# Optimization experiments

Measured on AMD Instinct MI355X. Metric: run time of the kernel, lower is better.

Reference implementation:

```python
import jax, jax.numpy as jnp
import numpy as np
import math

B, N0, IW, HW, OW, EG, DEPTH = 8, 16384, 128, 128, 2, 98304, 4
RATIO = 0.8


def setup_inputs() -> dict:
    key = jax.random.key(0)
    ks = list(jax.random.split(key, 40))
    inp = {
        "x": jax.random.normal(ks[0], (B, N0, IW), jnp.float32),
        "src": jax.random.randint(ks[1], (B, EG), 0, N0, jnp.int32),
        "dst": jax.random.randint(ks[2], (B, EG), 0, N0, jnp.int32),
    }
    def lin(k, fi, fo):
        return jax.random.normal(k, (fi, fo), jnp.float32) / np.sqrt(fi).astype(np.float32)
    j = 3
    for i in range(DEPTH):
        cin = IW if i == 0 else HW
        inp[f"c{i}_w1"] = lin(ks[j], cin, cin); j += 1
        inp[f"c{i}_b1"] = jnp.zeros((cin,), jnp.float32)
        inp[f"c{i}_w2"] = lin(ks[j], cin, HW); j += 1
        inp[f"c{i}_b2"] = jnp.zeros((HW,), jnp.float32)
        inp[f"p{i}_w"] = jax.random.normal(ks[j], (HW,), jnp.float32); j += 1
    inp["q1_w"] = lin(ks[j], 2 * HW, HW); j += 1
    inp["q1_b"] = jnp.zeros((HW,), jnp.float32)
    inp["q2_w"] = lin(ks[j], HW, HW // 2); j += 1
    inp["q2_b"] = jnp.zeros((HW // 2,), jnp.float32)
    inp["q3_w"] = lin(ks[j], HW // 2, OW); j += 1
    inp["q3_b"] = jnp.zeros((OW,), jnp.float32)
    return inp


def _forward(x, src, dst, conv_params, pool_ws, q1_w, q1_b, q2_w, q2_b, q3_w, q3_b):
    bidx = jnp.arange(B)[:, None]
    emask = jnp.ones(src.shape, x.dtype)  # edge validity mask (replaces PyG filter_adj)
    readouts = []
    for i in range(DEPTH):
        w1, b1, w2, b2 = conv_params[i]
        pw = pool_ws[i]
        # --- GINConv (eps=0, sum aggregation): MLP(x + sum_{j->i} x_j) ---
        msg = jnp.take_along_axis(x, src[:, :, None], axis=1) * emask[:, :, None]  # [B,E,C]
        agg = jnp.zeros_like(x).at[bidx, dst].add(msg)
        h = x + agg
        h = jax.nn.relu(h @ w1 + b1)
        x = jax.nn.relu(h @ w2 + b2)  # [B,n,HW]
        # --- TopKPooling(ratio=0.8, nonlinearity=tanh) ---
        n = x.shape[1]
        k = math.ceil(RATIO * n)
        score = jnp.tanh((x @ pw) / jnp.linalg.norm(pw))  # [B,n]
        vals, idx = jax.lax.top_k(score, k)  # per-graph top-k (descending)
        x = jnp.take_along_axis(x, idx[:, :, None], axis=1) * vals[:, :, None]  # [B,k,HW]
        # re-index edges: old node id -> new id (or -1 if dropped)
        mapping = jnp.full((B, n), -1, jnp.int32).at[bidx, idx].set(
            jnp.broadcast_to(jnp.arange(k, dtype=jnp.int32), (B, k)))
        nsrc = jnp.take_along_axis(mapping, src, axis=1)
        ndst = jnp.take_along_axis(mapping, dst, axis=1)
        valid = (nsrc >= 0) & (ndst >= 0) & (emask > 0)
        src = jnp.where(valid, nsrc, 0)
        dst = jnp.where(valid, ndst, 0)
        emask = valid.astype(x.dtype)
        # --- readout: [global_max_pool, global_mean_pool] ---
        readouts.append(jnp.concatenate([x.max(axis=1), x.mean(axis=1)], axis=1))
    r = readouts[0]
    for t in readouts[1:]:
        r = r + t  # sum over depth of stacked readouts
    # predictor (Dropout is identity in eval)
    h = jax.nn.relu(r @ q1_w + q1_b)
    h = jax.nn.relu(h @ q2_w + q2_b)
    return h @ q3_w + q3_b


def reference(x, src, dst,
              c0_w1, c0_b1, c0_w2, c0_b2, p0_w,
              c1_w1, c1_b1, c1_w2, c1_b2, p1_w,
              c2_w1, c2_b1, c2_w2, c2_b2, p2_w,
              c3_w1, c3_b1, c3_w2, c3_b2, p3_w,
              q1_w, q1_b, q2_w, q2_b, q3_w, q3_b):
    conv_params = [(c0_w1, c0_b1, c0_w2, c0_b2), (c1_w1, c1_b1, c1_w2, c1_b2),
                   (c2_w1, c2_b1, c2_w2, c2_b2), (c3_w1, c3_b1, c3_w2, c3_b2)]
    pool_ws = [p0_w, p1_w, p2_w, p3_w]
    return _forward(x, src, dst, conv_params, pool_ws, q1_w, q1_b, q2_w, q2_b, q3_w, q3_b)
```

## Files before the change

### kernel.cpp

```cpp
#include <hip/hip_runtime.h>
#include <math.h>

#define NB 8
#define N0 16384
#define NC 128
#define NE 98304

typedef unsigned short ushort_t;
using short8 = __attribute__((ext_vector_type(8))) short;
using f32x4 = __attribute__((ext_vector_type(4))) float;

__device__ __forceinline__ unsigned mono_u(float f) {
  unsigned u = __float_as_uint(f);
  return (u & 0x80000000u) ? ~u : (u | 0x80000000u);
}
__device__ __forceinline__ int f2ikey(float f) {
  int i = __float_as_int(f);
  return (i >= 0) ? i : (i ^ 0x7fffffff);
}
__device__ __forceinline__ float ikey2f(int k) {
  return __int_as_float(k >= 0 ? k : (k ^ 0x7fffffff));
}
__device__ __forceinline__ ushort_t f2bf_rne(float f) {
  unsigned u = __float_as_uint(f);
  unsigned r = u + 0x7fffu + ((u >> 16) & 1u);
  return (ushort_t)(r >> 16);
}
__device__ __forceinline__ int wscan_incl(int v, int lane) {
#pragma unroll
  for (int o = 1; o < 64; o <<= 1) {
    int u = __shfl_up(v, o);
    if (lane >= o) v += u;
  }
  return v;
}

__global__ void k_init(const int* __restrict__ src, const int* __restrict__ dst,
                       int* __restrict__ srcw, int* __restrict__ dstw,
                       int* __restrict__ cnt, int* __restrict__ maxbuf, float* __restrict__ sumbuf) {
  int stride = gridDim.x * blockDim.x;
  int i = blockIdx.x * blockDim.x + threadIdx.x;
  for (int j = i; j < NB * NE; j += stride) {
    int d = dst[j];
    srcw[j] = src[j];
    dstw[j] = d;
    atomicAdd(&cnt[(j / NE) * N0 + d], 1);
  }
  for (int j = i; j < 4 * NB * NC; j += stride) {
    maxbuf[j] = (int)0x80000000;
    sumbuf[j] = 0.f;
  }
}

__global__ void k_wprep(const float* __restrict__ W, ushort_t* __restrict__ Wt) {
  int id = blockIdx.x * blockDim.x + threadIdx.x;
  if (id >= NC * NC) return;
  int k = id >> 7, c = id & 127;
  Wt[c * NC + k] = f2bf_rne(W[id]);
}

__global__ __launch_bounds__(1024) void k_scan(int* __restrict__ cnt,
                                               int* __restrict__ offs, int* __restrict__ cursor) {
  __shared__ int wsum[16];
  int b = blockIdx.x, t = threadIdx.x, lane = t & 63, wid = t >> 6;
  int base = b * N0 + t * 16;
  int loc[16];
  int s = 0;
#pragma unroll
  for (int j = 0; j < 16; j++) { loc[j] = cnt[base + j]; s += loc[j]; cnt[base + j] = 0; }
  int incl = wscan_incl(s, lane);
  if (lane == 63) wsum[wid] = incl;
  __syncthreads();
  int woff = 0;
  for (int w = 0; w < wid; w++) woff += wsum[w];
  int excl = woff + incl - s;
#pragma unroll
  for (int j = 0; j < 16; j++) {
    offs[base + j] = excl;
    cursor[base + j] = excl;
    excl += loc[j];
  }
}

__global__ void k_fill(const int* __restrict__ srcw, const int* __restrict__ dstw,
                       int* __restrict__ cursor, int* __restrict__ elist) {
  int tot = NB * NE;
  for (int i = blockIdx.x * blockDim.x + threadIdx.x; i < tot; i += gridDim.x * blockDim.x) {
    int d = dstw[i];
    if (d < 0) continue;
    int b = i / NE;
    int pos = atomicAdd(&cursor[b * N0 + d], 1);
    elist[b * NE + pos] = srcw[i];
  }
}

__global__ void k_gather(const float* __restrict__ X, ushort_t* __restrict__ H,
                         const int* __restrict__ offs, const int* __restrict__ cend,
                         const int* __restrict__ elist, int n) {
  int b = blockIdx.x & 7;
  int chunk = blockIdx.x >> 3;
  int lane = threadIdx.x & 63, wid = threadIdx.x >> 6;
  int node = chunk * 4 + wid;
  if (node >= n) return;
  int off = offs[b * N0 + node];
  int deg = cend[b * N0 + node] - off;
  int h = lane >> 5, c4 = lane & 31;
  const float* Xb = X + (size_t)b * N0 * NC;

  float4 acc0 = make_float4(0.f, 0.f, 0.f, 0.f);
  float4 acc1 = make_float4(0.f, 0.f, 0.f, 0.f);
  if (h == 0) acc0 = *reinterpret_cast<const float4*>(&Xb[(size_t)node * NC + c4 * 4]);

  for (int base = 0; base < deg; base += 64) {
    int m = min(64, deg - base);
    int eid = (lane < m) ? elist[b * NE + off + base + lane] : 0;
    int j = 0;
    for (; j + 4 <= m; j += 4) {
      int s0 = __shfl(eid, j + h);
      int s1 = __shfl(eid, j + 2 + h);
      float4 v0 = *reinterpret_cast<const float4*>(&Xb[(size_t)s0 * NC + c4 * 4]);
      float4 v1 = *reinterpret_cast<const float4*>(&Xb[(size_t)s1 * NC + c4 * 4]);
      acc0.x += v0.x; acc0.y += v0.y; acc0.z += v0.z; acc0.w += v0.w;
      acc1.x += v1.x; acc1.y += v1.y; acc1.z += v1.z; acc1.w += v1.w;
    }
    if (j + 2 <= m) {
      int s0 = __shfl(eid, j + h);
      float4 v0 = *reinterpret_cast<const float4*>(&Xb[(size_t)s0 * NC + c4 * 4]);
      acc0.x += v0.x; acc0.y += v0.y; acc0.z += v0.z; acc0.w += v0.w;
      j += 2;
    }
    if (j < m) {
      int s0 = __shfl(eid, j);
      if (h == 0) {
        float4 v0 = *reinterpret_cast<const float4*>(&Xb[(size_t)s0 * NC + c4 * 4]);
        acc0.x += v0.x; acc0.y += v0.y; acc0.z += v0.z; acc0.w += v0.w;
      }
    }
  }
  acc0.x += acc1.x; acc0.y += acc1.y; acc0.z += acc1.z; acc0.w += acc1.w;
  acc0.x += __shfl_xor(acc0.x, 32);
  acc0.y += __shfl_xor(acc0.y, 32);
  acc0.z += __shfl_xor(acc0.z, 32);
  acc0.w += __shfl_xor(acc0.w, 32);
  if (h == 0) {
    unsigned p0 = (unsigned)f2bf_rne(acc0.x) | ((unsigned)f2bf_rne(acc0.y) << 16);
    unsigned p1 = (unsigned)f2bf_rne(acc0.z) | ((unsigned)f2bf_rne(acc0.w) << 16);
    *reinterpret_cast<uint2*>(&H[((size_t)b * N0 + node) * NC + c4 * 4]) = make_uint2(p0, p1);
  }
}

__global__ __launch_bounds__(256) void k_gin(const ushort_t* __restrict__ Xh,
                                             float* __restrict__ Xout,
                                             const ushort_t* __restrict__ W1t,
                                             const float* __restrict__ b1,
                                             const ushort_t* __restrict__ W2t,
                                             const float* __restrict__ b2,
                                             const float* __restrict__ pw,
                                             float* __restrict__ score, int n) {
  __shared__ ushort_t Ts[128 * 136];
  __shared__ ushort_t Wsh[128 * 136];
  int b = blockIdx.x & 7;
  int r0 = (blockIdx.x >> 3) * 128;
  int t = threadIdx.x;
  const ushort_t* Xg = Xh + (size_t)b * N0 * NC;

#pragma unroll
  for (int p = 0; p < 8; p++) {
    int id = t + p * 256;
    int row = id >> 4, seg = id & 15;
    short8 vh = (short8)0;
    if (r0 + row < n)
      vh = *reinterpret_cast<const short8*>(&Xg[(size_t)(r0 + row) * NC + seg * 8]);
    *reinterpret_cast<short8*>(&Ts[row * 136 + seg * 8]) = vh;
    *reinterpret_cast<short8*>(&Wsh[row * 136 + seg * 8]) =
        *reinterpret_cast<const short8*>(&W1t[row * NC + seg * 8]);
  }
  __syncthreads();

  int lane = t & 63, w = t >> 6;
  int li = lane & 15, lg = lane >> 4;
  int rbase = w * 32;

  f32x4 acc[2][8];
#pragma unroll
  for (int rt = 0; rt < 2; rt++)
#pragma unroll
    for (int ct = 0; ct < 8; ct++) acc[rt][ct] = (f32x4)0.f;

#pragma unroll
  for (int ks = 0; ks < 4; ks++) {
    short8 x0 = *reinterpret_cast<const short8*>(&Ts[(rbase + li) * 136 + ks * 32 + lg * 8]);
    short8 x1 = *reinterpret_cast<const short8*>(&Ts[(rbase + 16 + li) * 136 + ks * 32 + lg * 8]);
#pragma unroll
    for (int ct = 0; ct < 8; ct++) {
      short8 wf = *reinterpret_cast<const short8*>(&Wsh[(ct * 16 + li) * 136 + ks * 32 + lg * 8]);
      acc[0][ct] = __builtin_amdgcn_mfma_f32_16x16x32_bf16(wf, x0, acc[0][ct], 0, 0, 0);
      acc[1][ct] = __builtin_amdgcn_mfma_f32_16x16x32_bf16(wf, x1, acc[1][ct], 0, 0, 0);
    }
  }

#pragma unroll
  for (int rt = 0; rt < 2; rt++) {
    int row = rbase + rt * 16 + li;
#pragma unroll
    for (int ct = 0; ct < 8; ct++) {
      float4 bq = *reinterpret_cast<const float4*>(&b1[ct * 16 + lg * 4]);
      float o0 = fmaxf(acc[rt][ct][0] + bq.x, 0.f);
      float o1 = fmaxf(acc[rt][ct][1] + bq.y, 0.f);
      float o2 = fmaxf(acc[rt][ct][2] + bq.z, 0.f);
      float o3 = fmaxf(acc[rt][ct][3] + bq.w, 0.f);
      unsigned p0 = (unsigned)f2bf_rne(o0) | ((unsigned)f2bf_rne(o1) << 16);
      unsigned p1 = (unsigned)f2bf_rne(o2) | ((unsigned)f2bf_rne(o3) << 16);
      *reinterpret_cast<uint2*>(&Ts[row * 136 + ct * 16 + lg * 4]) = make_uint2(p0, p1);
    }
  }

  __syncthreads();
#pragma unroll
  for (int p = 0; p < 8; p++) {
    int id = t + p * 256;
    int row = id >> 4, seg = id & 15;
    *reinterpret_cast<short8*>(&Wsh[row * 136 + seg * 8]) =
        *reinterpret_cast<const short8*>(&W2t[row * NC + seg * 8]);
  }
  __syncthreads();

#pragma unroll
  for (int rt = 0; rt < 2; rt++)
#pragma unroll
    for (int ct = 0; ct < 8; ct++) acc[rt][ct] = (f32x4)0.f;

#pragma unroll
  for (int ks = 0; ks < 4; ks++) {
    short8 x0 = *reinterpret_cast<const short8*>(&Ts[(rbase + li) * 136 + ks * 32 + lg * 8]);
    short8 x1 = *reinterpret_cast<const short8*>(&Ts[(rbase + 16 + li) * 136 + ks * 32 + lg * 8]);
#pragma unroll
    for (int ct = 0; ct < 8; ct++) {
      short8 wf = *reinterpret_cast<const short8*>(&Wsh[(ct * 16 + li) * 136 + ks * 32 + lg * 8]);
      acc[0][ct] = __builtin_amdgcn_mfma_f32_16x16x32_bf16(wf, x0, acc[0][ct], 0, 0, 0);
      acc[1][ct] = __builtin_amdgcn_mfma_f32_16x16x32_bf16(wf, x1, acc[1][ct], 0, 0, 0);
    }
  }

  f32x4 pq[8];
  float psum = 0.f;
#pragma unroll
  for (int ct = 0; ct < 8; ct++) {
    pq[ct] = *reinterpret_cast<const f32x4*>(&pw[ct * 16 + lg * 4]);
    psum = fmaf(pq[ct][0], pq[ct][0], psum);
    psum = fmaf(pq[ct][1], pq[ct][1], psum);
    psum = fmaf(pq[ct][2], pq[ct][2], psum);
    psum = fmaf(pq[ct][3], pq[ct][3], psum);
  }
  psum += __shfl_xor(psum, 16);
  psum += __shfl_xor(psum, 32);
  float nrm = sqrtf(psum);

  float* Ob = Xout + (size_t)b * N0 * NC;
#pragma unroll
  for (int rt = 0; rt < 2; rt++) {
    int row = r0 + rbase + rt * 16 + li;
    bool ok = row < n;
    float dot = 0.f;
#pragma unroll
    for (int ct = 0; ct < 8; ct++) {
      float4 bq = *reinterpret_cast<const float4*>(&b2[ct * 16 + lg * 4]);
      float4 o;
      o.x = fmaxf(acc[rt][ct][0] + bq.x, 0.f);
      o.y = fmaxf(acc[rt][ct][1] + bq.y, 0.f);
      o.z = fmaxf(acc[rt][ct][2] + bq.z, 0.f);
      o.w = fmaxf(acc[rt][ct][3] + bq.w, 0.f);
      dot = fmaf(o.x, pq[ct][0], dot);
      dot = fmaf(o.y, pq[ct][1], dot);
      dot = fmaf(o.z, pq[ct][2], dot);
      dot = fmaf(o.w, pq[ct][3], dot);
      if (ok) *reinterpret_cast<float4*>(&Ob[(size_t)row * NC + ct * 16 + lg * 4]) = o;
    }
    dot += __shfl_xor(dot, 16);
    dot += __shfl_xor(dot, 32);
    if (lg == 0 && ok) score[b * N0 + row] = tanhf(dot / nrm);
  }
}

__global__ __launch_bounds__(1024) void k_select(const float* __restrict__ score,
                                                 unsigned* __restrict__ vstar, int* __restrict__ quota,
                                                 int* __restrict__ gcnt, int* __restrict__ tcnt,
                                                 int n, int k) {
  __shared__ int hist[256];
  __shared__ int ss[257];
  __shared__ unsigned s_pref;
  __shared__ int s_r, s_gt;
  int b = blockIdx.x, t = threadIdx.x, lane = t & 63;
  if (t == 0) { s_pref = 0u; s_r = k; s_gt = 0; }
  __syncthreads();
  for (int pass = 0; pass < 4; ++pass) {
    int shift = 24 - pass * 8;
    if (t < 256) hist[t] = 0;
    __syncthreads();
    unsigned pref = s_pref;
    unsigned pmask = (pass == 0) ? 0u : (0xFFFFFFFFu << (shift + 8));
    for (int j0 = 0; j0 < n; j0 += 1024) {
      int j = j0 + t;
      unsigned key = (j < n) ? mono_u(score[b * N0 + j]) : 0u;
      unsigned d = (key >> shift) & 255;
      int contrib = (j < n) && ((key & pmask) == pref);
      unsigned long long bal = __ballot(contrib);
      if (bal == 0) continue;
      int fl = __ffsll((long long)bal) - 1;
      unsigned dref = __shfl(d, fl);
      if (__all(!contrib || d == dref)) {
        if (lane == fl) atomicAdd(&hist[dref], (int)__popcll(bal));
      } else if (contrib) {
        atomicAdd(&hist[d], 1);
      }
    }
    __syncthreads();
    if (t < 256) ss[t] = hist[t];
    __syncthreads();
    for (int o = 1; o < 256; o <<= 1) {
      int v = 0;
      if (t < 256) v = (t + o < 256) ? ss[t + o] : 0;
      __syncthreads();
      if (t < 256) ss[t] += v;
      __syncthreads();
    }
    int r = s_r;
    __syncthreads();
    if (t < 256) {
      int nxt = (t == 255) ? 0 : ss[t + 1];
      if (ss[t] >= r && nxt < r) {
        s_gt += nxt;
        s_r = r - nxt;
        s_pref = pref | ((unsigned)t << shift);
      }
    }
    __syncthreads();
  }
  if (t == 0) {
    vstar[b] = s_pref;
    quota[b] = k - s_gt;
  }
  __syncthreads();
  unsigned vs = s_pref;
  int w = t >> 6;
  int g = 0, tt = 0;
  for (int it = 0; it < 16; ++it) {
    int j = w * 1024 + it * 64 + lane;
    unsigned key = (j < n) ? mono_u(score[b * N0 + j]) : 0u;
    g += (int)__popcll(__ballot((j < n) && (key > vs)));
    tt += (int)__popcll(__ballot((j < n) && (key == vs)));
  }
  if (lane == 0) { gcnt[b * 16 + w] = g; tcnt[b * 16 + w] = tt; }
}

__global__ __launch_bounds__(1024) void k_map_wr(const float* __restrict__ score,
                                                 const unsigned* __restrict__ vstar,
                                                 const int* __restrict__ quota,
                                                 const int* __restrict__ gcnt, const int* __restrict__ tcnt,
                                                 int* __restrict__ mp, int n) {
  __shared__ int wg[16], wt[16];
  __shared__ int s_gb, s_tb;
  int b = blockIdx.y, chunk = blockIdx.x, t = threadIdx.x;
  int lane = t & 63, wid = t >> 6;
  if (t == 0) {
    int gb = 0, tb = 0;
    for (int c = 0; c < chunk; c++) { gb += gcnt[b * 16 + c]; tb += tcnt[b * 16 + c]; }
    s_gb = gb; s_tb = tb;
  }
  int j = chunk * 1024 + t;
  unsigned vs = vstar[b];
  int q = quota[b];
  unsigned key = (j < n) ? mono_u(score[b * N0 + j]) : 0u;
  int gt = (j < n) && (key > vs);
  int tie = (j < n) && (key == vs);
  unsigned long long bg = __ballot(gt), bt = __ballot(tie);
  if (lane == 0) { wg[wid] = (int)__popcll(bg); wt[wid] = (int)__popcll(bt); }
  __syncthreads();
  if (j >= n) return;
  unsigned long long ltm = (lane == 63) ? ~0ull >> 1 : ((1ull << lane) - 1);
  int gloc = (int)__popcll(bg & ltm);
  int tloc = (int)__popcll(bt & ltm);
  for (int w = 0; w < 16; w++) {
    if (w < wid) { gloc += wg[w]; tloc += wt[w]; }
  }
  int tie_rank = s_tb + tloc;
  int sel = gt || (tie && tie_rank < q);
  int pos = s_gb + gloc + min(tie_rank, q);
  mp[b * N0 + j] = sel ? pos : -1;
}

__global__ __launch_bounds__(256) void k_compact(const float* __restrict__ Xin,
                                                 float* __restrict__ Xout,
                                                 const int* __restrict__ mp,
                                                 const float* __restrict__ score,
                                                 int* __restrict__ maxbuf, float* __restrict__ sumbuf,
                                                 int n) {
  __shared__ float smx[128], ssm[128];
  int b = blockIdx.x & 7;
  int base = (blockIdx.x >> 3) * 64;
  if (base >= n) return;
  int c = threadIdx.x & 127, h = threadIdx.x >> 7;
  float mx = -INFINITY, sm = 0.f;
  for (int r = h; r < 64; r += 2) {
    int node = base + r;
    if (node >= n) break;
    int m = mp[b * N0 + node];
    if (m < 0) continue;
    float val = score[b * N0 + node];
    float v = Xin[((size_t)b * N0 + node) * NC + c] * val;
    Xout[((size_t)b * N0 + m) * NC + c] = v;
    mx = fmaxf(mx, v);
    sm += v;
  }
  if (h) { smx[c] = mx; ssm[c] = sm; }
  __syncthreads();
  if (!h) {
    mx = fmaxf(mx, smx[c]);
    sm += ssm[c];
    atomicMax(&maxbuf[b * NC + c], f2ikey(mx));
    atomicAdd(&sumbuf[b * NC + c], sm);
  }
}

__global__ void k_remap(int* __restrict__ srcw, int* __restrict__ dstw,
                        const int* __restrict__ mp, int* __restrict__ cnt) {
  int b = blockIdx.x & 7;
  int bi = blockIdx.x >> 3;
  int nblk = gridDim.x >> 3;
  for (int e = bi * blockDim.x + threadIdx.x; e < NE; e += nblk * blockDim.x) {
    int i = b * NE + e;
    int d = dstw[i];
    if (d < 0) continue;
    int s = srcw[i];
    int ns = mp[b * N0 + s], nd = mp[b * N0 + d];
    if (ns >= 0 && nd >= 0) {
      srcw[i] = ns;
      dstw[i] = nd;
      atomicAdd(&cnt[b * N0 + nd], 1);
    } else {
      srcw[i] = 0;
      dstw[i] = -1;
    }
  }
}

__global__ __launch_bounds__(256) void k_pred(const int* __restrict__ maxbuf,
                                              const float* __restrict__ sumbuf,
                                              const float* __restrict__ q1w, const float* __restrict__ q1b,
                                              const float* __restrict__ q2w, const float* __restrict__ q2b,
                                              const float* __restrict__ q3w, const float* __restrict__ q3b,
                                              float* __restrict__ out) {
  __shared__ float rr[256], h1[128], h2[64];
  int b = blockIdx.x, t = threadIdx.x;
  const float kdiv[4] = {13108.f, 10487.f, 8390.f, 6712.f};
  float acc = 0.f;
#pragma unroll
  for (int d = 0; d < 4; d++) {
    if (t < 128) acc += ikey2f(maxbuf[d * NB * NC + b * NC + t]);
    else acc += sumbuf[d * NB * NC + b * NC + (t - 128)] / kdiv[d];
  }
  rr[t] = acc;
  __syncthreads();
  if (t < 128) {
    float s = q1b[t];
    for (int j = 0; j < 256; j++) s = fmaf(rr[j], q1w[j * 128 + t], s);
    h1[t] = fmaxf(s, 0.f);
  }
  __syncthreads();
  if (t < 64) {
    float s = q2b[t];
    for (int j = 0; j < 128; j++) s = fmaf(h1[j], q2w[j * 64 + t], s);
    h2[t] = fmaxf(s, 0.f);
  }
  __syncthreads();
  if (t < 2) {
    float s = q3b[t];
    for (int j = 0; j < 64; j++) s = fmaf(h2[j], q3w[j * 2 + t], s);
    out[b * 2 + t] = s;
  }
}

extern "C" void kernel_launch(void* const* d_in, const int* in_sizes, int n_in,
                              void* d_out, int out_size, void* d_ws, size_t ws_size,
                              hipStream_t stream) {
  const float* x = (const float*)d_in[0];
  const int* src = (const int*)d_in[1];
  const int* dst = (const int*)d_in[2];
  const float* q1w = (const float*)d_in[23];
  const float* q1b = (const float*)d_in[24];
  const float* q2w = (const float*)d_in[25];
  const float* q2b = (const float*)d_in[26];
  const float* q3w = (const float*)d_in[27];
  const float* q3b = (const float*)d_in[28];

  char* p = (char*)d_ws;
  auto alloc = [&](size_t bytes) {
    char* q = p;
    p += (bytes + 255) & ~(size_t)255;
    return q;
  };
  float* Xa = (float*)alloc((size_t)NB * N0 * NC * 4);
  float* Xb = (float*)alloc((size_t)NB * N0 * NC * 4);
  ushort_t* Xh = (ushort_t*)alloc((size_t)NB * N0 * NC * 2);
  int* srcw = (int*)alloc((size_t)NB * NE * 4);
  int* dstw = (int*)alloc((size_t)NB * NE * 4);
  int* elist = (int*)alloc((size_t)NB * NE * 4);
  int* cnt = (int*)alloc((size_t)NB * N0 * 4);
  int* offs = (int*)alloc((size_t)NB * N0 * 4);
  int* cursor = (int*)alloc((size_t)NB * N0 * 4);
  float* score = (float*)alloc((size_t)NB * N0 * 4);
  int* mp = (int*)alloc((size_t)NB * N0 * 4);
  unsigned* vstar = (unsigned*)alloc(256);
  int* quota = (int*)alloc(256);
  int* gcnt = (int*)alloc(NB * 16 * 4);
  int* tcnt = (int*)alloc(NB * 16 * 4);
  int* maxbuf = (int*)alloc(4 * NB * NC * 4);
  float* sumbuf = (float*)alloc(4 * NB * NC * 4);
  ushort_t* Wt_all = (ushort_t*)alloc((size_t)8 * NC * NC * 2);

  hipMemsetAsync(cnt, 0, (size_t)NB * N0 * 4, stream);
  k_init<<<2048, 256, 0, stream>>>(src, dst, srcw, dstw, cnt, maxbuf, sumbuf);
  for (int i = 0; i < 4; i++) {
    k_wprep<<<64, 256, 0, stream>>>((const float*)d_in[3 + i * 5 + 0], Wt_all + (size_t)(2 * i) * NC * NC);
    k_wprep<<<64, 256, 0, stream>>>((const float*)d_in[3 + i * 5 + 2], Wt_all + (size_t)(2 * i + 1) * NC * NC);
  }

  static const int NSv[4] = {16384, 13108, 10487, 8390};
  static const int KSv[4] = {13108, 10487, 8390, 6712};
  for (int i = 0; i < 4; i++) {
    int n = NSv[i], k = KSv[i];
    const float* b1 = (const float*)d_in[3 + i * 5 + 1];
    const float* b2 = (const float*)d_in[3 + i * 5 + 3];
    const float* pw = (const float*)d_in[3 + i * 5 + 4];
    const ushort_t* w1t = Wt_all + (size_t)(2 * i) * NC * NC;
    const ushort_t* w2t = Wt_all + (size_t)(2 * i + 1) * NC * NC;
    const float* cur = (i == 0) ? x : Xa;

    k_scan<<<NB, 1024, 0, stream>>>(cnt, offs, cursor);
    k_fill<<<1024, 256, 0, stream>>>(srcw, dstw, cursor, elist);

    k_gather<<<((n + 3) / 4) * 8, 256, 0, stream>>>(cur, Xh, offs, cursor, elist, n);

    k_gin<<<((n + 127) / 128) * 8, 256, 0, stream>>>(Xh, Xb, w1t, b1, w2t, b2, pw, score, n);

    k_select<<<NB, 1024, 0, stream>>>(score, vstar, quota, gcnt, tcnt, n, k);
    dim3 gm(16, NB);
    k_map_wr<<<gm, 1024, 0, stream>>>(score, vstar, quota, gcnt, tcnt, mp, n);

    k_compact<<<((n + 63) / 64) * 8, 256, 0, stream>>>(Xb, Xa, mp, score,
                                                       maxbuf + i * NB * NC, sumbuf + i * NB * NC, n);
    k_remap<<<512, 256, 0, stream>>>(srcw, dstw, mp, cnt);
  }

  k_pred<<<NB, 256, 0, stream>>>(maxbuf, sumbuf, q1w, q1b, q2w, q2b, q3w, q3b, (float*)d_out);
}
```

Baseline: 734.7 us.

## Fuse top-k select with map write, batch weight prep, prefetch W2 into registers

```diff
diff --git a/kernel.cpp b/kernel.cpp
--- a/kernel.cpp
+++ b/kernel.cpp
@@ -52,11 +52,25 @@
   }
 }
 
-__global__ void k_wprep(const float* __restrict__ W, ushort_t* __restrict__ Wt) {
+__global__ void k_wprep8(const float* w0, const float* w1, const float* w2, const float* w3,
+                         const float* w4, const float* w5, const float* w6, const float* w7,
+                         ushort_t* __restrict__ Wt_all) {
   int id = blockIdx.x * blockDim.x + threadIdx.x;
-  if (id >= NC * NC) return;
-  int k = id >> 7, c = id & 127;
-  Wt[c * NC + k] = f2bf_rne(W[id]);
+  if (id >= 8 * NC * NC) return;
+  int m = id >> 14, e = id & (NC * NC - 1);
+  const float* W;
+  switch (m) {
+    case 0: W = w0; break;
+    case 1: W = w1; break;
+    case 2: W = w2; break;
+    case 3: W = w3; break;
+    case 4: W = w4; break;
+    case 5: W = w5; break;
+    case 6: W = w6; break;
+    default: W = w7; break;
+  }
+  int kk = e >> 7, c = e & 127;
+  Wt_all[(size_t)m * NC * NC + c * NC + kk] = f2bf_rne(W[e]);
 }
 
 __global__ __launch_bounds__(1024) void k_scan(int* __restrict__ cnt,
@@ -164,6 +178,7 @@
   int t = threadIdx.x;
   const ushort_t* Xg = Xh + (size_t)b * N0 * NC;
 
+  short8 w2r[8];
 #pragma unroll
   for (int p = 0; p < 8; p++) {
     int id = t + p * 256;
@@ -174,6 +189,7 @@
     *reinterpret_cast<short8*>(&Ts[row * 136 + seg * 8]) = vh;
     *reinterpret_cast<short8*>(&Wsh[row * 136 + seg * 8]) =
         *reinterpret_cast<const short8*>(&W1t[row * NC + seg * 8]);
+    w2r[p] = *reinterpret_cast<const short8*>(&W2t[row * NC + seg * 8]);
   }
   __syncthreads();
 
@@ -220,8 +236,7 @@
   for (int p = 0; p < 8; p++) {
     int id = t + p * 256;
     int row = id >> 4, seg = id & 15;
-    *reinterpret_cast<short8*>(&Wsh[row * 136 + seg * 8]) =
-        *reinterpret_cast<const short8*>(&W2t[row * NC + seg * 8]);
+    *reinterpret_cast<short8*>(&Wsh[row * 136 + seg * 8]) = w2r[p];
   }
   __syncthreads();
 
@@ -282,15 +297,15 @@
   }
 }
 
-__global__ __launch_bounds__(1024) void k_select(const float* __restrict__ score,
-                                                 unsigned* __restrict__ vstar, int* __restrict__ quota,
-                                                 int* __restrict__ gcnt, int* __restrict__ tcnt,
-                                                 int n, int k) {
+__global__ __launch_bounds__(1024) void k_selmap(const float* __restrict__ score,
+                                                 int* __restrict__ mp, int n, int k) {
   __shared__ int hist[256];
   __shared__ int ss[257];
+  __shared__ int sgc[16], stc[16];
+  __shared__ int wg[16], wt[16];
   __shared__ unsigned s_pref;
   __shared__ int s_r, s_gt;
-  int b = blockIdx.x, t = threadIdx.x, lane = t & 63;
+  int b = blockIdx.x, t = threadIdx.x, lane = t & 63, wid = t >> 6;
   if (t == 0) { s_pref = 0u; s_r = k; s_gt = 0; }
   __syncthreads();
   for (int pass = 0; pass < 4; ++pass) {
@@ -336,57 +351,44 @@
     }
     __syncthreads();
   }
-  if (t == 0) {
-    vstar[b] = s_pref;
-    quota[b] = k - s_gt;
-  }
-  __syncthreads();
   unsigned vs = s_pref;
-  int w = t >> 6;
-  int g = 0, tt = 0;
-  for (int it = 0; it < 16; ++it) {
-    int j = w * 1024 + it * 64 + lane;
+  int q = k - s_gt;
+  {
+    int g = 0, tt = 0;
+    for (int it = 0; it < 16; ++it) {
+      int j = wid * 1024 + it * 64 + lane;
+      unsigned key = (j < n) ? mono_u(score[b * N0 + j]) : 0u;
+      g += (int)__popcll(__ballot((j < n) && (key > vs)));
+      tt += (int)__popcll(__ballot((j < n) && (key == vs)));
+    }
+    if (lane == 0) { sgc[wid] = g; stc[wid] = tt; }
+  }
+  __syncthreads();
+  int gb = 0, tb = 0;
+  for (int c = 0; c < 16; ++c) {
+    int j = c * 1024 + t;
     unsigned key = (j < n) ? mono_u(score[b * N0 + j]) : 0u;
-    g += (int)__popcll(__ballot((j < n) && (key > vs)));
-    tt += (int)__popcll(__ballot((j < n) && (key == vs)));
-  }
-  if (lane == 0) { gcnt[b * 16 + w] = g; tcnt[b * 16 + w] = tt; }
-}
-
-__global__ __launch_bounds__(1024) void k_map_wr(const float* __restrict__ score,
-                                                 const unsigned* __restrict__ vstar,
-                                                 const int* __restrict__ quota,
-                                                 const int* __restrict__ gcnt, const int* __restrict__ tcnt,
-                                                 int* __restrict__ mp, int n) {
-  __shared__ int wg[16], wt[16];
-  __shared__ int s_gb, s_tb;
-  int b = blockIdx.y, chunk = blockIdx.x, t = threadIdx.x;
-  int lane = t & 63, wid = t >> 6;
-  if (t == 0) {
-    int gb = 0, tb = 0;
-    for (int c = 0; c < chunk; c++) { gb += gcnt[b * 16 + c]; tb += tcnt[b * 16 + c]; }
-    s_gb = gb; s_tb = tb;
-  }
-  int j = chunk * 1024 + t;
-  unsigned vs = vstar[b];
-  int q = quota[b];
-  unsigned key = (j < n) ? mono_u(score[b * N0 + j]) : 0u;
-  int gt = (j < n) && (key > vs);
-  int tie = (j < n) && (key == vs);
-  unsigned long long bg = __ballot(gt), bt = __ballot(tie);
-  if (lane == 0) { wg[wid] = (int)__popcll(bg); wt[wid] = (int)__popcll(bt); }
-  __syncthreads();
-  if (j >= n) return;
-  unsigned long long ltm = (lane == 63) ? ~0ull >> 1 : ((1ull << lane) - 1);
-  int gloc = (int)__popcll(bg & ltm);
-  int tloc = (int)__popcll(bt & ltm);
-  for (int w = 0; w < 16; w++) {
-    if (w < wid) { gloc += wg[w]; tloc += wt[w]; }
-  }
-  int tie_rank = s_tb + tloc;
-  int sel = gt || (tie && tie_rank < q);
-  int pos = s_gb + gloc + min(tie_rank, q);
-  mp[b * N0 + j] = sel ? pos : -1;
+    int gt = (j < n) && (key > vs);
+    int tie = (j < n) && (key == vs);
+    unsigned long long bg = __ballot(gt), bt = __ballot(tie);
+    if (lane == 0) { wg[wid] = (int)__popcll(bg); wt[wid] = (int)__popcll(bt); }
+    __syncthreads();
+    if (j < n) {
+      unsigned long long ltm = (lane == 63) ? ~0ull >> 1 : ((1ull << lane) - 1);
+      int gloc = (int)__popcll(bg & ltm);
+      int tloc = (int)__popcll(bt & ltm);
+      for (int w = 0; w < 16; w++) {
+        if (w < wid) { gloc += wg[w]; tloc += wt[w]; }
+      }
+      int tie_rank = tb + tloc;
+      int sel = gt || (tie && tie_rank < q);
+      int pos = gb + gloc + min(tie_rank, q);
+      mp[b * N0 + j] = sel ? pos : -1;
+    }
+    gb += sgc[c];
+    tb += stc[c];
+    __syncthreads();
+  }
 }
 
 __global__ __launch_bounds__(256) void k_compact(const float* __restrict__ Xin,
@@ -510,20 +512,17 @@
   int* cursor = (int*)alloc((size_t)NB * N0 * 4);
   float* score = (float*)alloc((size_t)NB * N0 * 4);
   int* mp = (int*)alloc((size_t)NB * N0 * 4);
-  unsigned* vstar = (unsigned*)alloc(256);
-  int* quota = (int*)alloc(256);
-  int* gcnt = (int*)alloc(NB * 16 * 4);
-  int* tcnt = (int*)alloc(NB * 16 * 4);
   int* maxbuf = (int*)alloc(4 * NB * NC * 4);
   float* sumbuf = (float*)alloc(4 * NB * NC * 4);
   ushort_t* Wt_all = (ushort_t*)alloc((size_t)8 * NC * NC * 2);
 
   hipMemsetAsync(cnt, 0, (size_t)NB * N0 * 4, stream);
   k_init<<<2048, 256, 0, stream>>>(src, dst, srcw, dstw, cnt, maxbuf, sumbuf);
-  for (int i = 0; i < 4; i++) {
-    k_wprep<<<64, 256, 0, stream>>>((const float*)d_in[3 + i * 5 + 0], Wt_all + (size_t)(2 * i) * NC * NC);
-    k_wprep<<<64, 256, 0, stream>>>((const float*)d_in[3 + i * 5 + 2], Wt_all + (size_t)(2 * i + 1) * NC * NC);
-  }
+  k_wprep8<<<512, 256, 0, stream>>>(
+      (const float*)d_in[3], (const float*)d_in[5],
+      (const float*)d_in[8], (const float*)d_in[10],
+      (const float*)d_in[13], (const float*)d_in[15],
+      (const float*)d_in[18], (const float*)d_in[20], Wt_all);
 
   static const int NSv[4] = {16384, 13108, 10487, 8390};
   static const int KSv[4] = {13108, 10487, 8390, 6712};
@@ -543,9 +542,7 @@
 
     k_gin<<<((n + 127) / 128) * 8, 256, 0, stream>>>(Xh, Xb, w1t, b1, w2t, b2, pw, score, n);
 
-    k_select<<<NB, 1024, 0, stream>>>(score, vstar, quota, gcnt, tcnt, n, k);
-    dim3 gm(16, NB);
-    k_map_wr<<<gm, 1024, 0, stream>>>(score, vstar, quota, gcnt, tcnt, mp, n);
+    k_selmap<<<NB, 1024, 0, stream>>>(score, mp, n, k);
 
     k_compact<<<((n + 63) / 64) * 8, 256, 0, stream>>>(Xb, Xa, mp, score,
                                                        maxbuf + i * NB * NC, sumbuf + i * NB * NC, n);
```

Measured after the change: 744.5 us, median of 4. About the same (+1.3%).
